# Kernel optimization log

Measured on AMD Instinct MI355X. Metric: run time of the kernel, lower is better.

## Reference

```python
import jax, jax.numpy as jnp
import numpy as np

N = 100000
E = 1000000
IN_C, HID, OUT_C = 128, 128, 40
DROPOUT_P = 0.5
BN_EPS = 1e-5


def setup_inputs() -> dict:
    key = jax.random.key(0)
    ks = jax.random.split(key, 10)
    x = jax.random.normal(ks[0], (N, IN_C), dtype=jnp.float32)
    edge_index = jax.random.randint(ks[1], (2, E), 0, N, dtype=jnp.int32)

    def glorot(k, fan_in, fan_out):
        lim = np.sqrt(6.0 / (fan_in + fan_out)).astype(np.float32)
        return jax.random.uniform(k, (fan_in, fan_out), jnp.float32, -lim, lim)

    return {
        "x": x,
        "edge_index": edge_index,
        "W1": glorot(ks[2], IN_C, HID), "b1": jnp.zeros((HID,), jnp.float32),
        "g1": jnp.ones((HID,), jnp.float32), "be1": jnp.zeros((HID,), jnp.float32),
        "W2": glorot(ks[3], HID, HID), "b2": jnp.zeros((HID,), jnp.float32),
        "g2": jnp.ones((HID,), jnp.float32), "be2": jnp.zeros((HID,), jnp.float32),
        "W3": glorot(ks[4], HID, OUT_C), "b3": jnp.zeros((OUT_C,), jnp.float32),
    }


def _deg_inv_sqrt(dst):
    # degree from destination nodes, +1 for the added self loop (PyG gcn_norm)
    deg = jax.ops.segment_sum(jnp.ones((E,), jnp.float32), dst, num_segments=N) + 1.0
    return jax.lax.rsqrt(deg)


def _gcn_conv(h, W, b, src, dst, dinv):
    # h: [N, Cin] -> [N, Cout]; y = D^-1/2 (A + I) D^-1/2 (h W) + b
    hw = h @ W
    norm = dinv[src] * dinv[dst]                      # [E]
    msg = hw[src] * norm[:, None]                     # [E, Cout] gather (memory-bound)
    agg = jax.ops.segment_sum(msg, dst, num_segments=N)
    agg = agg + hw * (dinv * dinv)[:, None]           # self-loop contribution
    return agg + b


def _batchnorm(h, gamma, beta):
    mu = jnp.mean(h, axis=0)
    var = jnp.mean(jnp.square(h - mu), axis=0)        # biased, training mode
    return (h - mu) * jax.lax.rsqrt(var + BN_EPS) * gamma + beta


def _dropout(h, key):
    keep = jax.random.bernoulli(key, 1.0 - DROPOUT_P, h.shape)
    return jnp.where(keep, h / (1.0 - DROPOUT_P), 0.0)


def reference(x, edge_index, W1, b1, g1, be1, W2, b2, g2, be2, W3, b3):
    src, dst = edge_index[0], edge_index[1]
    dinv = _deg_inv_sqrt(dst)
    dk = jax.random.split(jax.random.key(42), 2)

    h = _gcn_conv(x, W1, b1, src, dst, dinv)
    h = _dropout(jax.nn.relu(_batchnorm(h, g1, be1)), dk[0])

    h = _gcn_conv(h, W2, b2, src, dst, dinv)
    h = _dropout(jax.nn.relu(_batchnorm(h, g2, be2)), dk[1])

    h = _gcn_conv(h, W3, b3, src, dst, dinv)
    return jax.nn.log_softmax(h, axis=1)
```

## Files before the change

kernel.cpp:

```cpp
#include <hip/hip_runtime.h>
#include <math.h>

typedef __attribute__((ext_vector_type(8))) short bf16x8;
typedef __attribute__((ext_vector_type(4))) float f32x4;

__device__ __forceinline__ float bfbits2f(unsigned short b){
  return __uint_as_float(((unsigned)b) << 16);
}
__device__ __forceinline__ unsigned short f2bfbits(float f){
  unsigned u = __float_as_uint(f);
  unsigned r = u + 0x7fffu + ((u >> 16) & 1u);
  return (unsigned short)(r >> 16);
}

__host__ __device__ __forceinline__ unsigned rotl32(unsigned v, int d){
  return (v << d) | (v >> (32 - d));
}
__host__ __device__ __forceinline__ void tf2x32(unsigned k0, unsigned k1,
                                                unsigned c0, unsigned c1,
                                                unsigned &o0, unsigned &o1)
{
  unsigned ks2 = k0 ^ k1 ^ 0x1BD11BDAu;
  unsigned x0 = c0 + k0, x1 = c1 + k1;
#define TFR(r) x0 += x1; x1 = rotl32(x1, r); x1 ^= x0;
  TFR(13) TFR(15) TFR(26) TFR(6)
  x0 += k1;  x1 += ks2 + 1u;
  TFR(17) TFR(29) TFR(16) TFR(24)
  x0 += ks2; x1 += k0 + 2u;
  TFR(13) TFR(15) TFR(26) TFR(6)
  x0 += k0;  x1 += k1 + 3u;
  TFR(17) TFR(29) TFR(16) TFR(24)
  x0 += k1;  x1 += ks2 + 4u;
  TFR(13) TFR(15) TFR(26) TFR(6)
  x0 += ks2; x1 += k0 + 5u;
#undef TFR
  o0 = x0; o1 = x1;
}

__device__ __forceinline__ void gen_mask(unsigned* __restrict__ mask,
                                         unsigned mk0, unsigned mk1,
                                         int g, int total, int M)
{
  for (int wi = g; wi < M; wi += total){
    unsigned bits = 0u;
    #pragma unroll 4
    for (int j = 0; j < 32; j++){
      unsigned w0, w1;
      tf2x32(mk0, mk1, 0u, (unsigned)wi * 32u + (unsigned)j, w0, w1);
      bits |= (((w0 ^ w1) >> 31) << j);
    }
    mask[wi] = bits;
  }
}

__global__ __launch_bounds__(256) void k_countpos(const int* __restrict__ dst,
                                                  int* __restrict__ cnt,
                                                  int* __restrict__ pos, int E,
                                                  unsigned* __restrict__ mask,
                                                  unsigned mk0, unsigned mk1, int M)
{
  int g = blockIdx.x * 256 + threadIdx.x;
  int base = g * 4;
  if (base + 3 < E){
    int4 d = ((const int4*)dst)[g];
    int4 p;
    p.x = atomicAdd(&cnt[d.x], 1);
    p.y = atomicAdd(&cnt[d.y], 1);
    p.z = atomicAdd(&cnt[d.z], 1);
    p.w = atomicAdd(&cnt[d.w], 1);
    ((int4*)pos)[g] = p;
  } else {
    for (int j = 0; j < 4; j++){
      int e = base + j;
      if (e < E) pos[e] = atomicAdd(&cnt[dst[e]], 1);
    }
  }
  gen_mask(mask, mk0, mk1, g, gridDim.x * 256, M);
}

__global__ __launch_bounds__(256) void k_blocksum(const int* __restrict__ cnt,
                                                  int* __restrict__ bsum, int N)
{
  __shared__ int sh[256];
  int t = threadIdx.x;
  int base = blockIdx.x * 1024 + t * 4;
  int s = 0;
  #pragma unroll
  for (int j = 0; j < 4; j++){ int i = base + j; if (i < N) s += cnt[i]; }
  sh[t] = s; __syncthreads();
  for (int off = 128; off; off >>= 1){
    if (t < off) sh[t] += sh[t + off];
    __syncthreads();
  }
  if (t == 0) bsum[blockIdx.x] = sh[0];
}

__global__ __launch_bounds__(256) void k_scansums(const int* __restrict__ bsum,
                                                  int* __restrict__ boff,
                                                  int* __restrict__ rowstart,
                                                  int NB, int N)
{
  __shared__ int sh[256];
  int t = threadIdx.x;
  int v = (t < NB) ? bsum[t] : 0;
  sh[t] = v; __syncthreads();
  for (int off = 1; off < 256; off <<= 1){
    int x = sh[t];
    int y = (t >= off) ? sh[t - off] : 0;
    __syncthreads();
    sh[t] = x + y;
    __syncthreads();
  }
  if (t < NB) boff[t] = sh[t] - v;
  if (t == NB - 1) rowstart[N] = sh[t];
}

__global__ __launch_bounds__(256) void k_scanfinal(const int* __restrict__ cnt,
                                                   const int* __restrict__ boff,
                                                   int* __restrict__ rowstart,
                                                   float* __restrict__ dinv, int N)
{
  __shared__ int sh[256];
  int t = threadIdx.x;
  int base = blockIdx.x * 1024 + t * 4;
  int c0 = 0, c1 = 0, c2 = 0, c3 = 0;
  if (base + 0 < N) c0 = cnt[base + 0];
  if (base + 1 < N) c1 = cnt[base + 1];
  if (base + 2 < N) c2 = cnt[base + 2];
  if (base + 3 < N) c3 = cnt[base + 3];
  int s = c0 + c1 + c2 + c3;
  sh[t] = s; __syncthreads();
  for (int off = 1; off < 256; off <<= 1){
    int x = sh[t];
    int y = (t >= off) ? sh[t - off] : 0;
    __syncthreads();
    sh[t] = x + y;
    __syncthreads();
  }
  int excl = sh[t] - s + boff[blockIdx.x];
  if (base + 0 < N){ rowstart[base+0] = excl;          dinv[base+0] = rsqrtf((float)c0 + 1.f); }
  if (base + 1 < N){ rowstart[base+1] = excl+c0;       dinv[base+1] = rsqrtf((float)c1 + 1.f); }
  if (base + 2 < N){ rowstart[base+2] = excl+c0+c1;    dinv[base+2] = rsqrtf((float)c2 + 1.f); }
  if (base + 3 < N){ rowstart[base+3] = excl+c0+c1+c2; dinv[base+3] = rsqrtf((float)c3 + 1.f); }
}

__global__ __launch_bounds__(256) void k_fill(const int* __restrict__ src,
                                              const int* __restrict__ dst,
                                              const int* __restrict__ pos,
                                              const int* __restrict__ rowstart,
                                              int* __restrict__ csr, int E,
                                              unsigned* __restrict__ mask,
                                              unsigned mk0, unsigned mk1, int M)
{
  int g = blockIdx.x * 256 + threadIdx.x;
  int base = g * 4;
  if (base + 3 < E){
    int4 d = ((const int4*)dst)[g];
    int4 p = ((const int4*)pos)[g];
    int4 s = ((const int4*)src)[g];
    int r0 = rowstart[d.x], r1 = rowstart[d.y], r2 = rowstart[d.z], r3 = rowstart[d.w];
    csr[r0 + p.x] = s.x;
    csr[r1 + p.y] = s.y;
    csr[r2 + p.z] = s.z;
    csr[r3 + p.w] = s.w;
  } else {
    for (int j = 0; j < 4; j++){
      int e = base + j;
      if (e < E) csr[rowstart[dst[e]] + pos[e]] = src[e];
    }
  }
  gen_mask(mask, mk0, mk1, g, gridDim.x * 256, M);
}

__global__ __launch_bounds__(256) void k_wt(const float* __restrict__ W1,
                                            const float* __restrict__ W2,
                                            const float* __restrict__ W3,
                                            unsigned short* __restrict__ WT1,
                                            unsigned short* __restrict__ WT2,
                                            unsigned short* __restrict__ WT3)
{
  const float* W; unsigned short* WT; int Cout, Cpad;
  if (blockIdx.x == 0){ W = W1; WT = WT1; Cout = 128; Cpad = 128; }
  else if (blockIdx.x == 1){ W = W2; WT = WT2; Cout = 128; Cpad = 128; }
  else { W = W3; WT = WT3; Cout = 40; Cpad = 48; }
  int tot = Cpad * 128;
  for (int i = threadIdx.x; i < tot; i += 256){
    int n = i >> 7, k = i & 127;
    float v = (n < Cout) ? W[k * Cout + n] : 0.f;
    WT[i] = f2bfbits(v);
  }
}

template<int NT, int MODE>
__global__ __launch_bounds__(256) void k_gemm_mfma(const void* __restrict__ Ap,
                                                   const unsigned short* __restrict__ WT,
                                                   const float* __restrict__ dinv,
                                                   const float* __restrict__ stats,
                                                   const float* __restrict__ g,
                                                   const float* __restrict__ be,
                                                   const unsigned* __restrict__ mask,
                                                   float invN,
                                                   unsigned short* __restrict__ outb,
                                                   int N, int Cout)
{
  __shared__ uint4 Wl4[NT * 16 * 16];
  __shared__ uint4 Al4[64 * 16];
  __shared__ float bnS[128], bnB[128];
  const int t = threadIdx.x;
  const int w = t >> 6, l = t & 63;
  const long rb0 = (long)blockIdx.x * 64;
  const int wrow0 = w * 16;

  uint4 rawU[4];
  float4 rawF[4][2];
  unsigned mword[4];
  int rr[4], cc[4];
  bool inr[4];
  #pragma unroll
  for (int i = 0; i < 4; i++){
    int idx = i * 64 + l;
    int r = idx >> 4, c = idx & 15;
    long grow = rb0 + wrow0 + r;
    rr[i] = r; cc[i] = c; inr[i] = (grow < N);
    if (inr[i]){
      if (MODE == 0){
        const float* ap = (const float*)Ap + grow * 128 + c * 8;
        rawF[i][0] = *(const float4*)ap;
        rawF[i][1] = *(const float4*)(ap + 4);
      } else {
        rawU[i] = *(const uint4*)((const unsigned short*)Ap + grow * 128 + c * 8);
        mword[i] = mask[((unsigned)grow << 2) + (c >> 2)];
      }
    }
  }

  {
    const uint4* s4 = (const uint4*)WT;
    const int tot = NT * 16 * 16;
    for (int i = t; i < tot; i += 256){
      int n = i >> 4, c = i & 15;
      Wl4[n * 16 + (c ^ (n & 15))] = s4[i];
    }
  }
  if (MODE == 2 && t < 128){
    float ss = 0.f, qq = 0.f;
    #pragma unroll
    for (int i = 0; i < 16; i++){
      ss += stats[i * 256 + t];
      qq += stats[i * 256 + 128 + t];
    }
    float mean = ss * invN;
    float var = fmaxf(qq * invN - mean * mean, 0.f);
    float rstd = rsqrtf(var + 1e-5f);
    float sc = g[t] * rstd;
    bnS[t] = sc;
    bnB[t] = be[t] - mean * sc;
  }
  __syncthreads();

  #pragma unroll
  for (int i = 0; i < 4; i++){
    uint4 chunk = make_uint4(0u, 0u, 0u, 0u);
    if (inr[i]){
      if (MODE == 0){
        chunk.x = (unsigned)f2bfbits(rawF[i][0].x) | ((unsigned)f2bfbits(rawF[i][0].y) << 16);
        chunk.y = (unsigned)f2bfbits(rawF[i][0].z) | ((unsigned)f2bfbits(rawF[i][0].w) << 16);
        chunk.z = (unsigned)f2bfbits(rawF[i][1].x) | ((unsigned)f2bfbits(rawF[i][1].y) << 16);
        chunk.w = (unsigned)f2bfbits(rawF[i][1].z) | ((unsigned)f2bfbits(rawF[i][1].w) << 16);
      } else {
        unsigned mb = mword[i] >> ((cc[i] & 3) * 8);
        const unsigned* rw = &rawU[i].x;
        unsigned* cw = &chunk.x;
        #pragma unroll
        for (int h = 0; h < 4; h++){
          int ch = cc[i] * 8 + 2 * h;
          float f0 = bfbits2f((unsigned short)(rw[h] & 0xffffu));
          float f1 = bfbits2f((unsigned short)(rw[h] >> 16));
          f0 = fmaxf(fmaf(f0, bnS[ch],     bnB[ch]),     0.f);
          f1 = fmaxf(fmaf(f1, bnS[ch + 1], bnB[ch + 1]), 0.f);
          f0 = ((mb >> (2 * h))     & 1u) ? 0.f : f0 * 2.f;
          f1 = ((mb >> (2 * h + 1)) & 1u) ? 0.f : f1 * 2.f;
          cw[h] = (unsigned)f2bfbits(f0) | ((unsigned)f2bfbits(f1) << 16);
        }
      }
    }
    Al4[(wrow0 + rr[i]) * 16 + (cc[i] ^ rr[i])] = chunk;
  }

  const int lm = l & 15, q = l >> 4;

  f32x4 acc[NT];
  #pragma unroll
  for (int nt = 0; nt < NT; nt++){
    acc[nt][0] = 0.f; acc[nt][1] = 0.f; acc[nt][2] = 0.f; acc[nt][3] = 0.f;
  }

  #pragma unroll
  for (int kt = 0; kt < 4; kt++){
    const int x = kt * 4 + q;
    bf16x8 a = *(const bf16x8*)&Al4[(wrow0 + lm) * 16 + (x ^ lm)];
    #pragma unroll
    for (int nt = 0; nt < NT; nt++){
      int brow = nt * 16 + lm;
      bf16x8 b = *(const bf16x8*)&Wl4[brow * 16 + (x ^ (brow & 15))];
      acc[nt] = __builtin_amdgcn_mfma_f32_16x16x32_bf16(a, b, acc[nt], 0, 0, 0);
    }
  }

  #pragma unroll
  for (int r = 0; r < 4; r++){
    long row = rb0 + wrow0 + q * 4 + r;
    if (row < N){
      float dv = dinv[row];
      #pragma unroll
      for (int nt = 0; nt < NT; nt++){
        int col = nt * 16 + lm;
        if (col < Cout)
          outb[row * Cout + col] = f2bfbits(acc[nt][r] * dv);
      }
    }
  }
}

#define ACC8(U) do{ uint4 _u = (U); \
  a0 += bfbits2f((unsigned short)(_u.x & 0xffffu)); \
  a1 += bfbits2f((unsigned short)(_u.x >> 16)); \
  a2 += bfbits2f((unsigned short)(_u.y & 0xffffu)); \
  a3 += bfbits2f((unsigned short)(_u.y >> 16)); \
  a4 += bfbits2f((unsigned short)(_u.z & 0xffffu)); \
  a5 += bfbits2f((unsigned short)(_u.z >> 16)); \
  a6 += bfbits2f((unsigned short)(_u.w & 0xffffu)); \
  a7 += bfbits2f((unsigned short)(_u.w >> 16)); }while(0)

__global__ __launch_bounds__(256) void k_agg128s(const unsigned short* __restrict__ hw,
                                                 const int* __restrict__ rs,
                                                 const int* __restrict__ csr,
                                                 const float* __restrict__ dinv,
                                                 unsigned short* __restrict__ outb,
                                                 float* __restrict__ stats,
                                                 int N)
{
  const int l = threadIdx.x;
  const int ns = l >> 4;
  const int sl = l & 15;
  const int ty = threadIdx.y;
  const int grp = ty * 4 + ns;
  const uint4* h16 = (const uint4*)hw;
  const int base = blockIdx.x * 32;

  float s0=0.f,s1=0.f,s2=0.f,s3=0.f,s4=0.f,s5=0.f,s6=0.f,s7=0.f;
  float q0=0.f,q1=0.f,q2=0.f,q3=0.f,q4=0.f,q5=0.f,q6=0.f,q7=0.f;

  #pragma unroll 1
  for (int it = 0; it < 2; it++){
    int v = base + it * 16 + grp;
    if (v < N){
      float a0=0.f,a1=0.f,a2=0.f,a3=0.f,a4=0.f,a5=0.f,a6=0.f,a7=0.f;
      ACC8(h16[(size_t)v * 16 + sl]);
      int e0 = rs[v], e1 = rs[v + 1];
      int i = e0;
      for (; i + 4 <= e1; i += 4){
        int sa = csr[i], sb = csr[i+1], sc = csr[i+2], sd = csr[i+3];
        uint4 m0 = h16[(size_t)sa * 16 + sl];
        uint4 m1 = h16[(size_t)sb * 16 + sl];
        uint4 m2 = h16[(size_t)sc * 16 + sl];
        uint4 m3 = h16[(size_t)sd * 16 + sl];
        ACC8(m0); ACC8(m1); ACC8(m2); ACC8(m3);
      }
      for (; i < e1; i++){
        ACC8(h16[(size_t)csr[i] * 16 + sl]);
      }
      float dv = dinv[v];
      a0*=dv; a1*=dv; a2*=dv; a3*=dv; a4*=dv; a5*=dv; a6*=dv; a7*=dv;
      uint4 o;
      o.x = (unsigned)f2bfbits(a0) | ((unsigned)f2bfbits(a1) << 16);
      o.y = (unsigned)f2bfbits(a2) | ((unsigned)f2bfbits(a3) << 16);
      o.z = (unsigned)f2bfbits(a4) | ((unsigned)f2bfbits(a5) << 16);
      o.w = (unsigned)f2bfbits(a6) | ((unsigned)f2bfbits(a7) << 16);
      ((uint4*)outb)[(size_t)v * 16 + sl] = o;
      s0+=a0; q0=fmaf(a0,a0,q0);  s1+=a1; q1=fmaf(a1,a1,q1);
      s2+=a2; q2=fmaf(a2,a2,q2);  s3+=a3; q3=fmaf(a3,a3,q3);
      s4+=a4; q4=fmaf(a4,a4,q4);  s5+=a5; q5=fmaf(a5,a5,q5);
      s6+=a6; q6=fmaf(a6,a6,q6);  s7+=a7; q7=fmaf(a7,a7,q7);
    }
  }

  __shared__ float shS[16][128], shQ[16][128];
  *(float4*)&shS[grp][sl * 8]     = make_float4(s0, s1, s2, s3);
  *(float4*)&shS[grp][sl * 8 + 4] = make_float4(s4, s5, s6, s7);
  *(float4*)&shQ[grp][sl * 8]     = make_float4(q0, q1, q2, q3);
  *(float4*)&shQ[grp][sl * 8 + 4] = make_float4(q4, q5, q6, q7);
  __syncthreads();
  int t = ty * 64 + threadIdx.x;
  if (t < 128){
    float ss = 0.f, qq = 0.f;
    #pragma unroll
    for (int g2 = 0; g2 < 16; g2++){ ss += shS[g2][t]; qq += shQ[g2][t]; }
    float* dstat = stats + (blockIdx.x & 15) * 256;
    atomicAdd(&dstat[t], ss);
    atomicAdd(&dstat[128 + t], qq);
  }
}

#define ACC2(U) do{ unsigned _u = (U); \
  acx += bfbits2f((unsigned short)(_u & 0xffffu)); \
  acy += bfbits2f((unsigned short)(_u >> 16)); }while(0)

__global__ __launch_bounds__(256) void k_agg40lsm(const unsigned short* __restrict__ hw,
                                                  const int* __restrict__ rs,
                                                  const int* __restrict__ csr,
                                                  const float* __restrict__ dinv,
                                                  const float* __restrict__ b3,
                                                  float* __restrict__ out, int N)
{
  int half = (threadIdx.x >> 5) & 1;
  int sl = threadIdx.x & 31;
  int v = blockIdx.x * 8 + threadIdx.y * 2 + half;
  bool nact = (v < N);
  bool act = nact && (sl < 20);
  const unsigned* h2 = (const unsigned*)hw;
  float acx = 0.f, acy = 0.f, dv = 1.f;
  if (act){
    dv = dinv[v];
    ACC2(h2[(size_t)v * 20 + sl]);
    int e0 = rs[v], e1 = rs[v + 1];
    int i = e0;
    for (; i + 4 <= e1; i += 4){
      int s0 = csr[i], s1 = csr[i+1], s2 = csr[i+2], s3 = csr[i+3];
      unsigned u0 = h2[(size_t)s0 * 20 + sl];
      unsigned u1 = h2[(size_t)s1 * 20 + sl];
      unsigned u2 = h2[(size_t)s2 * 20 + sl];
      unsigned u3 = h2[(size_t)s3 * 20 + sl];
      ACC2(u0); ACC2(u1); ACC2(u2); ACC2(u3);
    }
    for (; i < e1; i++){
      ACC2(h2[(size_t)csr[i] * 20 + sl]);
    }
  }
  float x0 = act ? fmaf(acx, dv, b3[2 * sl])     : -INFINITY;
  float x1 = act ? fmaf(acy, dv, b3[2 * sl + 1]) : -INFINITY;
  float m = fmaxf(x0, x1);
  #pragma unroll
  for (int off = 16; off; off >>= 1) m = fmaxf(m, __shfl_xor(m, off, 32));
  float e = act ? (expf(x0 - m) + expf(x1 - m)) : 0.f;
  #pragma unroll
  for (int off = 16; off; off >>= 1) e += __shfl_xor(e, off, 32);
  float lse = m + logf(e);
  if (act){
    float2 o; o.x = x0 - lse; o.y = x1 - lse;
    *reinterpret_cast<float2*>(out + (size_t)v * 40 + 2 * sl) = o;
  }
}

extern "C" void kernel_launch(void* const* d_in, const int* in_sizes, int n_in,
                              void* d_out, int out_size, void* d_ws, size_t ws_size,
                              hipStream_t stream)
{
  const float* x  = (const float*)d_in[0];
  const int* ei   = (const int*)d_in[1];
  const float* W1 = (const float*)d_in[2];
  const float* g1 = (const float*)d_in[4];
  const float* be1= (const float*)d_in[5];
  const float* W2 = (const float*)d_in[6];
  const float* g2 = (const float*)d_in[8];
  const float* be2= (const float*)d_in[9];
  const float* W3 = (const float*)d_in[10];
  const float* b3 = (const float*)d_in[11];
  float* out = (float*)d_out;

  const int N = in_sizes[0] / 128;
  const int E = in_sizes[1] / 2;
  const int* srcv = ei;
  const int* dstv = ei + E;

  char* ws = (char*)d_ws;
  size_t off = 0;
  auto take = [&](size_t bytes) -> void* {
    void* p = ws + off;
    off = (off + bytes + 255) & ~(size_t)255;
    return p;
  };
  int*   cnt      = (int*)  take((size_t)N * 4);
  int*   pos      = (int*)  take((size_t)E * 4);
  int*   rowstart = (int*)  take((size_t)(N + 1) * 4);
  int*   csr      = (int*)  take((size_t)E * 4);
  float* dinv     = (float*)take((size_t)N * 4);
  int*   bsum     = (int*)  take(256 * 4);
  int*   boff     = (int*)  take(256 * 4);
  float* stats    = (float*)take(16 * 256 * 4);
  unsigned* mask1 = (unsigned*)take((size_t)N * 4 * 4);
  unsigned* mask2 = (unsigned*)take((size_t)N * 4 * 4);
  unsigned short* WT1 = (unsigned short*)take(128 * 128 * 2);
  unsigned short* WT2 = (unsigned short*)take(128 * 128 * 2);
  unsigned short* WT3 = (unsigned short*)take(48 * 128 * 2);
  unsigned short* bufX = (unsigned short*)take((size_t)N * 128 * 2);
  unsigned short* bufY = (unsigned short*)take((size_t)N * 128 * 2);
  (void)ws_size; (void)n_in; (void)out_size;

  unsigned l1k0, l1k1, l2k0, l2k1;
  tf2x32(0u, 42u, 0u, 0u, l1k0, l1k1);
  tf2x32(0u, 42u, 0u, 1u, l2k0, l2k1);

  const float invN = 1.0f / (float)N;
  const int M = N * 4;
  const int NB = (N + 1023) / 1024;
  dim3 wgrid8((N + 7) / 8), wblk(64, 4);
  dim3 wgrid32((N + 31) / 32);
  const int ggrid = (N + 63) / 64;
  const int egrid = (E + 1023) / 1024;

  hipMemsetAsync(cnt, 0, (size_t)N * 4, stream);
  k_countpos<<<egrid, 256, 0, stream>>>(dstv, cnt, pos, E, mask1, l1k0, l1k1, M);
  k_blocksum<<<NB, 256, 0, stream>>>(cnt, bsum, N);
  k_scansums<<<1, 256, 0, stream>>>(bsum, boff, rowstart, NB, N);
  k_scanfinal<<<NB, 256, 0, stream>>>(cnt, boff, rowstart, dinv, N);
  k_fill<<<egrid, 256, 0, stream>>>(srcv, dstv, pos, rowstart, csr, E, mask2, l2k0, l2k1, M);
  k_wt<<<3, 256, 0, stream>>>(W1, W2, W3, WT1, WT2, WT3);

  k_gemm_mfma<8, 0><<<ggrid, 256, 0, stream>>>(x, WT1, dinv,
      nullptr, nullptr, nullptr, nullptr, invN, bufX, N, 128);
  hipMemsetAsync(stats, 0, 16 * 256 * 4, stream);
  k_agg128s<<<wgrid32, wblk, 0, stream>>>(bufX, rowstart, csr, dinv, bufY, stats, N);

  k_gemm_mfma<8, 2><<<ggrid, 256, 0, stream>>>(bufY, WT2, dinv,
      stats, g1, be1, mask1, invN, bufX, N, 128);
  hipMemsetAsync(stats, 0, 16 * 256 * 4, stream);
  k_agg128s<<<wgrid32, wblk, 0, stream>>>(bufX, rowstart, csr, dinv, bufY, stats, N);

  k_gemm_mfma<3, 2><<<ggrid, 256, 0, stream>>>(bufY, WT3, dinv,
      stats, g2, be2, mask2, invN, bufX, N, 40);
  k_agg40lsm<<<wgrid8, wblk, 0, stream>>>(bufX, rowstart, csr, dinv, b3, out, N);
}
```

Baseline: 415.6 us.

## Move dropout mask generation into aggregation kernels and widen final aggregation lanes

Threefry dropout mask generation moves out of the atomic-heavy CSR build kernels and into the memory-bound 128-wide aggregation kernels. The ALU-heavy hashing can then overlap with gather latency. The two per-layer stats memsets are merged into one upfront memset over two separate buffers. The final 40-channel aggregation plus log-softmax now uses 10 of 16 lanes per node with 8-byte loads instead of 20 of 32 lanes with 4-byte loads, which packs more nodes per block. The risk is longer aggregation kernels and extra register pressure from mask generation.

```diff
diff --git a/kernel.cpp b/kernel.cpp
--- a/kernel.cpp
+++ b/kernel.cpp
@@ -55,9 +55,7 @@
 
 __global__ __launch_bounds__(256) void k_countpos(const int* __restrict__ dst,
                                                   int* __restrict__ cnt,
-                                                  int* __restrict__ pos, int E,
-                                                  unsigned* __restrict__ mask,
-                                                  unsigned mk0, unsigned mk1, int M)
+                                                  int* __restrict__ pos, int E)
 {
   int g = blockIdx.x * 256 + threadIdx.x;
   int base = g * 4;
@@ -75,7 +73,6 @@
       if (e < E) pos[e] = atomicAdd(&cnt[dst[e]], 1);
     }
   }
-  gen_mask(mask, mk0, mk1, g, gridDim.x * 256, M);
 }
 
 __global__ __launch_bounds__(256) void k_blocksum(const int* __restrict__ cnt,
@@ -148,9 +145,7 @@
                                               const int* __restrict__ dst,
                                               const int* __restrict__ pos,
                                               const int* __restrict__ rowstart,
-                                              int* __restrict__ csr, int E,
-                                              unsigned* __restrict__ mask,
-                                              unsigned mk0, unsigned mk1, int M)
+                                              int* __restrict__ csr, int E)
 {
   int g = blockIdx.x * 256 + threadIdx.x;
   int base = g * 4;
@@ -169,7 +164,6 @@
       if (e < E) csr[rowstart[dst[e]] + pos[e]] = src[e];
     }
   }
-  gen_mask(mask, mk0, mk1, g, gridDim.x * 256, M);
 }
 
 __global__ __launch_bounds__(256) void k_wt(const float* __restrict__ W1,
@@ -338,6 +332,8 @@
                                                  const float* __restrict__ dinv,
                                                  unsigned short* __restrict__ outb,
                                                  float* __restrict__ stats,
+                                                 unsigned* __restrict__ mask,
+                                                 unsigned mk0, unsigned mk1, int M,
                                                  int N)
 {
   const int l = threadIdx.x;
@@ -347,6 +343,8 @@
   const int grp = ty * 4 + ns;
   const uint4* h16 = (const uint4*)hw;
   const int base = blockIdx.x * 32;
+
+  gen_mask(mask, mk0, mk1, blockIdx.x * 256 + ty * 64 + l, gridDim.x * 256, M);
 
   float s0=0.f,s1=0.f,s2=0.f,s3=0.f,s4=0.f,s5=0.f,s6=0.f,s7=0.f;
   float q0=0.f,q1=0.f,q2=0.f,q3=0.f,q4=0.f,q5=0.f,q6=0.f,q7=0.f;
@@ -402,10 +400,6 @@
   }
 }
 
-#define ACC2(U) do{ unsigned _u = (U); \
-  acx += bfbits2f((unsigned short)(_u & 0xffffu)); \
-  acy += bfbits2f((unsigned short)(_u >> 16)); }while(0)
-
 __global__ __launch_bounds__(256) void k_agg40lsm(const unsigned short* __restrict__ hw,
                                                   const int* __restrict__ rs,
                                                   const int* __restrict__ csr,
@@ -413,42 +407,54 @@
                                                   const float* __restrict__ b3,
                                                   float* __restrict__ out, int N)
 {
-  int half = (threadIdx.x >> 5) & 1;
-  int sl = threadIdx.x & 31;
-  int v = blockIdx.x * 8 + threadIdx.y * 2 + half;
-  bool nact = (v < N);
-  bool act = nact && (sl < 20);
-  const unsigned* h2 = (const unsigned*)hw;
-  float acx = 0.f, acy = 0.f, dv = 1.f;
+  const int l = threadIdx.x;
+  const int ns = l >> 4, sl = l & 15;
+  const int v = blockIdx.x * 16 + threadIdx.y * 4 + ns;
+  const bool act = (v < N) && (sl < 10);
+  const uint2* h2 = (const uint2*)hw;
+  float a0 = 0.f, a1 = 0.f, a2 = 0.f, a3 = 0.f, dv = 1.f;
   if (act){
     dv = dinv[v];
-    ACC2(h2[(size_t)v * 20 + sl]);
+    uint2 u = h2[(size_t)v * 10 + sl];
+    a0 = bfbits2f((unsigned short)(u.x & 0xffffu));
+    a1 = bfbits2f((unsigned short)(u.x >> 16));
+    a2 = bfbits2f((unsigned short)(u.y & 0xffffu));
+    a3 = bfbits2f((unsigned short)(u.y >> 16));
     int e0 = rs[v], e1 = rs[v + 1];
     int i = e0;
+#define ACCU2(U) do{ uint2 _u = (U); \
+    a0 += bfbits2f((unsigned short)(_u.x & 0xffffu)); \
+    a1 += bfbits2f((unsigned short)(_u.x >> 16)); \
+    a2 += bfbits2f((unsigned short)(_u.y & 0xffffu)); \
+    a3 += bfbits2f((unsigned short)(_u.y >> 16)); }while(0)
     for (; i + 4 <= e1; i += 4){
-      int s0 = csr[i], s1 = csr[i+1], s2 = csr[i+2], s3 = csr[i+3];
-      unsigned u0 = h2[(size_t)s0 * 20 + sl];
-      unsigned u1 = h2[(size_t)s1 * 20 + sl];
-      unsigned u2 = h2[(size_t)s2 * 20 + sl];
-      unsigned u3 = h2[(size_t)s3 * 20 + sl];
-      ACC2(u0); ACC2(u1); ACC2(u2); ACC2(u3);
+      int sa = csr[i], sb = csr[i+1], sc = csr[i+2], sd = csr[i+3];
+      uint2 m0 = h2[(size_t)sa * 10 + sl];
+      uint2 m1 = h2[(size_t)sb * 10 + sl];
+      uint2 m2 = h2[(size_t)sc * 10 + sl];
+      uint2 m3 = h2[(size_t)sd * 10 + sl];
+      ACCU2(m0); ACCU2(m1); ACCU2(m2); ACCU2(m3);
     }
     for (; i < e1; i++){
-      ACC2(h2[(size_t)csr[i] * 20 + sl]);
-    }
-  }
-  float x0 = act ? fmaf(acx, dv, b3[2 * sl])     : -INFINITY;
-  float x1 = act ? fmaf(acy, dv, b3[2 * sl + 1]) : -INFINITY;
-  float m = fmaxf(x0, x1);
-  #pragma unroll
-  for (int off = 16; off; off >>= 1) m = fmaxf(m, __shfl_xor(m, off, 32));
-  float e = act ? (expf(x0 - m) + expf(x1 - m)) : 0.f;
-  #pragma unroll
-  for (int off = 16; off; off >>= 1) e += __shfl_xor(e, off, 32);
+      ACCU2(h2[(size_t)csr[i] * 10 + sl]);
+    }
+#undef ACCU2
+  }
+  float x0 = act ? fmaf(a0, dv, b3[sl * 4 + 0]) : -INFINITY;
+  float x1 = act ? fmaf(a1, dv, b3[sl * 4 + 1]) : -INFINITY;
+  float x2 = act ? fmaf(a2, dv, b3[sl * 4 + 2]) : -INFINITY;
+  float x3 = act ? fmaf(a3, dv, b3[sl * 4 + 3]) : -INFINITY;
+  float m = fmaxf(fmaxf(x0, x1), fmaxf(x2, x3));
+  #pragma unroll
+  for (int off = 8; off; off >>= 1) m = fmaxf(m, __shfl_xor(m, off, 16));
+  float e = act ? (expf(x0 - m) + expf(x1 - m) + expf(x2 - m) + expf(x3 - m)) : 0.f;
+  #pragma unroll
+  for (int off = 8; off; off >>= 1) e += __shfl_xor(e, off, 16);
   float lse = m + logf(e);
   if (act){
-    float2 o; o.x = x0 - lse; o.y = x1 - lse;
-    *reinterpret_cast<float2*>(out + (size_t)v * 40 + 2 * sl) = o;
+    float4 o;
+    o.x = x0 - lse; o.y = x1 - lse; o.z = x2 - lse; o.w = x3 - lse;
+    *reinterpret_cast<float4*>(out + (size_t)v * 40 + sl * 4) = o;
   }
 }
 
@@ -487,7 +493,8 @@
   float* dinv     = (float*)take((size_t)N * 4);
   int*   bsum     = (int*)  take(256 * 4);
   int*   boff     = (int*)  take(256 * 4);
-  float* stats    = (float*)take(16 * 256 * 4);
+  float* stats1   = (float*)take(2 * 16 * 256 * 4);
+  float* stats2   = stats1 + 16 * 256;
   unsigned* mask1 = (unsigned*)take((size_t)N * 4 * 4);
   unsigned* mask2 = (unsigned*)take((size_t)N * 4 * 4);
   unsigned short* WT1 = (unsigned short*)take(128 * 128 * 2);
@@ -504,30 +511,32 @@
   const float invN = 1.0f / (float)N;
   const int M = N * 4;
   const int NB = (N + 1023) / 1024;
-  dim3 wgrid8((N + 7) / 8), wblk(64, 4);
+  dim3 wblk(64, 4);
+  dim3 wgrid16((N + 15) / 16);
   dim3 wgrid32((N + 31) / 32);
   const int ggrid = (N + 63) / 64;
   const int egrid = (E + 1023) / 1024;
 
   hipMemsetAsync(cnt, 0, (size_t)N * 4, stream);
-  k_countpos<<<egrid, 256, 0, stream>>>(dstv, cnt, pos, E, mask1, l1k0, l1k1, M);
+  hipMemsetAsync(stats1, 0, 2 * 16 * 256 * 4, stream);
+  k_countpos<<<egrid, 256, 0, stream>>>(dstv, cnt, pos, E);
   k_blocksum<<<NB, 256, 0, stream>>>(cnt, bsum, N);
   k_scansums<<<1, 256, 0, stream>>>(bsum, boff, rowstart, NB, N);
   k_scanfinal<<<NB, 256, 0, stream>>>(cnt, boff, rowstart, dinv, N);
-  k_fill<<<egrid, 256, 0, stream>>>(srcv, dstv, pos, rowstart, csr, E, mask2, l2k0, l2k1, M);
+  k_fill<<<egrid, 256, 0, stream>>>(srcv, dstv, pos, rowstart, csr, E);
   k_wt<<<3, 256, 0, stream>>>(W1, W2, W3, WT1, WT2, WT3);
 
   k_gemm_mfma<8, 0><<<ggrid, 256, 0, stream>>>(x, WT1, dinv,
       nullptr, nullptr, nullptr, nullptr, invN, bufX, N, 128);
-  hipMemsetAsync(stats, 0, 16 * 256 * 4, stream);
-  k_agg128s<<<wgrid32, wblk, 0, stream>>>(bufX, rowstart, csr, dinv, bufY, stats, N);
+  k_agg128s<<<wgrid32, wblk, 0, stream>>>(bufX, rowstart, csr, dinv, bufY, stats1,
+      mask1, l1k0, l1k1, M, N);
 
   k_gemm_mfma<8, 2><<<ggrid, 256, 0, stream>>>(bufY, WT2, dinv,
-      stats, g1, be1, mask1, invN, bufX, N, 128);
-  hipMemsetAsync(stats, 0, 16 * 256 * 4, stream);
-  k_agg128s<<<wgrid32, wblk, 0, stream>>>(bufX, rowstart, csr, dinv, bufY, stats, N);
+      stats1, g1, be1, mask1, invN, bufX, N, 128);
+  k_agg128s<<<wgrid32, wblk, 0, stream>>>(bufX, rowstart, csr, dinv, bufY, stats2,
+      mask2, l2k0, l2k1, M, N);
 
   k_gemm_mfma<3, 2><<<ggrid, 256, 0, stream>>>(bufY, WT3, dinv,
-      stats, g2, be2, mask2, invN, bufX, N, 40);
-  k_agg40lsm<<<wgrid8, wblk, 0, stream>>>(bufX, rowstart, csr, dinv, b3, out, N);
-}
+      stats2, g2, be2, mask2, invN, bufX, N, 40);
+  k_agg40lsm<<<wgrid16, wblk, 0, stream>>>(bufX, rowstart, csr, dinv, b3, out, N);
+}
```

Result: faster. 401.0 us (-3.5%).
